# Kernel optimization log

Hardware: AMD Instinct MI355X
Metric: run time of the kernel (lower is better)

Reference implementation:

```python
import jax, jax.numpy as jnp
import numpy as np

L = 8          # fixed number of instance labels (0 = background), all assumed present
DV = 0.5       # delta_v
DD = 1.5       # delta_d
LOSS_WEIGHT = 1.0


def _safe_norm(x, axis):
    sq = jnp.sum(x * x, axis=axis)
    pos = sq > 0
    return jnp.sqrt(jnp.where(pos, sq, 1.0)) * pos.astype(x.dtype)


def _per_image(emb, inst, kern, tmask):
    # emb: [D,H,W], inst: [H,W] int, kern/tmask: [H,W] float
    D, H, W = emb.shape
    HW = H * W
    tm = (tmask > 0.5).astype(inst.dtype)
    kb = (kern > 0.5).astype(inst.dtype)
    inst = inst * tm
    inst_k = (inst * kb).reshape(-1)          # kernel-region labels
    inst_f = inst.reshape(-1)                 # full-region labels
    emb_f = emb.reshape(D, -1).T              # [HW, D]

    # --- generate_coef: first/second occurrence (row-major) of each label ---
    flat = jnp.arange(HW)
    eq = inst_f[None, :] == jnp.arange(L)[:, None]          # [L, HW]
    idxs = jnp.where(eq, flat[None, :], HW)
    first = jnp.min(idxs, axis=1)
    second = jnp.min(jnp.where(idxs == first[:, None], HW, idxs), axis=1)
    first = jnp.minimum(first, HW - 1)
    second = jnp.minimum(second, HW - 1)
    r0, c0 = first // W, first % W
    r1, c1 = second // W, second % W
    # pos_id = (tmp[0,0], tmp[1,0], tmp[0,-1], tmp[1,-1]) as in the source
    pos = jnp.stack([r0, r1, c0, c1], axis=1).astype(jnp.float32)  # [L,4]
    diag = jnp.sqrt(jnp.float32(H * H + W * W))
    coef_diag = jnp.exp(jnp.sqrt((pos[:, 0] - pos[:, 2]) ** 2 +
                                 (pos[:, 1] - pos[:, 3]) ** 2) / diag / 2.0)
    zmask = (jnp.arange(L) > 0).astype(jnp.float32)          # skip label 0
    coef_diag = coef_diag * zmask
    s = pos[:, 0] + pos[:, 2]
    t = pos[:, 1] + pos[:, 3]
    dp = jnp.sqrt((s[:, None] - s[None, :]) ** 2 + (t[:, None] - t[None, :]) ** 2)
    coef_off = 1.0 - 20.0 * jnp.exp(-4.0 - 2.5 * dp / diag)
    eye = jnp.eye(L, dtype=bool)
    coef = jnp.where(eye, coef_diag[:, None], coef_off)
    coef = coef * zmask[:, None] * zmask[None, :]

    # --- per-label kernel means (segment mean) ---
    ones = jnp.ones((HW,), jnp.float32)
    cnt_k = jax.ops.segment_sum(ones, inst_k, num_segments=L)
    mean = jax.ops.segment_sum(emb_f, inst_k, num_segments=L)
    mean = mean / jnp.maximum(cnt_k, 1.0)[:, None]           # [L, D]
    mean = mean * zmask[:, None]

    # --- l_agg: per-pixel distance to own-label mean, segment-mean per label ---
    mean_px = mean[inst_f]                                   # [HW, D] gather
    dist = _safe_norm(emb_f - mean_px, axis=1)
    cd_px = coef_diag[inst_f]
    val = jnp.log(jax.nn.relu(cd_px * dist - DV) ** 2 + 1.0)
    cnt = jax.ops.segment_sum(ones, inst_f, num_segments=L)
    l_agg_per = jax.ops.segment_sum(val, inst_f, num_segments=L) / jnp.maximum(cnt, 1.0)
    l_agg = jnp.mean(l_agg_per[1:])

    # --- l_dis: coefficient-weighted pairwise hinge between means ---
    Dn = _safe_norm(mean[:, None, :] - mean[None, :, :], axis=-1)  # [L, L]
    pm = (~eye) & (zmask[:, None] > 0) & (zmask[None, :] > 0)
    vals = jnp.log(jax.nn.relu(2.0 * DD - coef * Dn) ** 2 + 1.0)
    l_dis = jnp.sum(jnp.where(pm, vals, 0.0)) / ((L - 1) * (L - 2))

    # --- l_reg ---
    l_reg = jnp.mean(jnp.log(_safe_norm(mean, axis=1) + 1.0)) * 0.001
    return l_agg + l_dis + l_reg


def reference(emb, instance, kernel, training_mask, bboxes):
    # bboxes is accepted but unused, matching the original forward_single
    loss_batch = jax.vmap(_per_image)(emb, instance, kernel, training_mask)
    return LOSS_WEIGHT * jnp.mean(loss_batch)


def setup_inputs() -> dict:
    key = jax.random.key(0)
    k1, k2, k3, k4, k5 = jax.random.split(key, 5)
    B, D, H, W = 8, 4, 640, 640
    emb = jax.random.normal(k1, (B, D, H, W), dtype=jnp.float32)
    instance = jax.random.randint(k2, (B, H, W), 0, L, dtype=jnp.int32)
    kernel = jax.random.uniform(k3, (B, H, W), dtype=jnp.float32)
    training_mask = jax.random.uniform(k4, (B, H, W), dtype=jnp.float32)
    bboxes = jax.random.uniform(k5, (B, 10, 4), dtype=jnp.float32)
    return {"emb": emb, "instance": instance, "kernel": kernel,
            "training_mask": training_mask, "bboxes": bboxes}
```

## Files before the change

### kernel.cpp

```cpp
#include <hip/hip_runtime.h>

#define B_    8
#define D_    4
#define H_    640
#define W_    640
#define HW_   (H_ * W_)
#define L_    8
#define NL    (L_ - 1)
#define BLOCK 256
#define VITER 4
#define PXB   (BLOCK * 4 * VITER)
#define GRIDX (HW_ / PXB)

__device__ __forceinline__ void gatom_add(float* p, float v) {
    unsafeAtomicAdd(p, v);
}

__global__ void k_init(int* ib) {
    int t = threadIdx.x;
    if (t < 128) ib[t] = HW_;
    ib[128 + t] = 0;
    if (t < 137) ib[384 + t] = 0;
}

__global__ __attribute__((amdgpu_flat_work_group_size(BLOCK, BLOCK),
                          amdgpu_waves_per_eu(4, 8)))
void k_pass1(
        const float* __restrict__ emb, const int* __restrict__ inst,
        const float* __restrict__ kern, const float* __restrict__ tmask,
        int* __restrict__ firstIdx, int* __restrict__ secondIdx,
        int* __restrict__ cntf_i, int* __restrict__ cntk_i,
        float* __restrict__ sumemb, uint2* __restrict__ lblpack) {
    __shared__ int   sCnt[L_];
    __shared__ float sSum[L_ * D_];
    __shared__ int   sM1[L_], sM2[L_];

    const int tid  = threadIdx.x;
    const int lane = tid & 63;
    if (tid < L_) { sCnt[tid] = 0; sM1[tid] = HW_; sM2[tid] = HW_; }
    if (tid < L_ * D_) sSum[tid] = 0.f;
    __syncthreads();

    const int b = blockIdx.y;
    const int blockbase = blockIdx.x * PXB;
    const float* embb = emb + (size_t)b * D_ * HW_;
    const int base = b * HW_;
    const int o0 = blockbase + tid * 4;

    int4 LB[VITER]; float4 TM[VITER], KN[VITER];
    #pragma unroll
    for (int it = 0; it < VITER; ++it) {
        const int o = o0 + it * (BLOCK * 4);
        LB[it] = *(const int4*)  (inst  + base + o);
        TM[it] = *(const float4*)(tmask + base + o);
        KN[it] = *(const float4*)(kern  + base + o);
    }
    float4 E[2][2][D_];
    #pragma unroll
    for (int s = 0; s < 2; ++s)
        #pragma unroll
        for (int d = 0; d < D_; ++d)
            E[0][s][d] = *(const float4*)(embb + d * HW_ + o0 + s * (BLOCK * 4));

    int bp0 = 0, bp1 = 0, bp2 = 0, km = 0;
    unsigned int lpLo = 0, lpHi = 0;
    #pragma unroll
    for (int it = 0; it < VITER; ++it) {
        const int*   labA = (const int*)&LB[it];
        const float* tmA  = (const float*)&TM[it];
        const float* knA  = (const float*)&KN[it];
        #pragma unroll
        for (int c = 0; c < 4; ++c) {
            const int px = it * 4 + c;
            const int lf  = (tmA[c] > 0.5f) ? labA[c] : 0;
            const bool kb = (knA[c] > 0.5f);
            bp0 |= (lf & 1) << px;
            bp1 |= ((lf >> 1) & 1) << px;
            bp2 |= ((lf >> 2) & 1) << px;
            km  |= (kb ? 1 : 0) << px;
            if (px < 8) lpLo |= (unsigned int)lf << (4 * px);
            else        lpHi |= (unsigned int)lf << (4 * (px - 8));
        }
    }

    lblpack[(size_t)(b * GRIDX + blockIdx.x) * BLOCK + tid] = make_uint2(lpLo, lpHi);

    #pragma unroll
    for (int s = 0; s < 2; ++s)
        #pragma unroll
        for (int d = 0; d < D_; ++d)
            E[1][s][d] = *(const float4*)(embb + d * HW_ + o0 + (2 + s) * (BLOCK * 4));

    float sm[NL][D_];
    #pragma unroll
    for (int l = 0; l < NL; ++l)
        #pragma unroll
        for (int d = 0; d < D_; ++d) sm[l][d] = 0.f;

    #pragma unroll
    for (int half = 0; half < 2; ++half) {
        const unsigned int lp = half ? lpHi : lpLo;
        #pragma unroll
        for (int s = 0; s < 2; ++s) {
            const float* e0A = (const float*)&E[half][s][0];
            const float* e1A = (const float*)&E[half][s][1];
            const float* e2A = (const float*)&E[half][s][2];
            const float* e3A = (const float*)&E[half][s][3];
            #pragma unroll
            for (int c = 0; c < 4; ++c) {
                const int px  = half * 8 + s * 4 + c;
                const int nib = s * 4 + c;
                const int lf  = (int)((lp >> (4 * nib)) & 7u);
                const int lfk = ((km >> px) & 1) ? lf : 0;
                #pragma unroll
                for (int l = 1; l < L_; ++l) {
                    const float mk = (lfk == l) ? 1.0f : 0.0f;
                    sm[l - 1][0] += mk * e0A[c];
                    sm[l - 1][1] += mk * e1A[c];
                    sm[l - 1][2] += mk * e2A[c];
                    sm[l - 1][3] += mk * e3A[c];
                }
            }
        }
    }

    const int nb0 = ~bp0, nb1 = ~bp1, nb2 = ~bp2;
    int cnt[NL], m1[NL], m2[NL];
    #pragma unroll
    for (int l = 1; l < L_; ++l) {
        const int k = l - 1;
        int h = ((l & 1) ? bp0 : nb0) & ((l & 2) ? bp1 : nb1) & ((l & 4) ? bp2 : nb2);
        h &= 0xFFFF;
        cnt[k] = (__popc(h) << 16) | __popc(h & km);
        const int h2 = h & (h - 1);
        const int p1 = __ffs(h) - 1;
        const int p2 = __ffs(h2) - 1;
        m1[k] = h  ? (o0 + (p1 >> 2) * (BLOCK * 4) + (p1 & 3)) : HW_;
        m2[k] = h2 ? (o0 + (p2 >> 2) * (BLOCK * 4) + (p2 & 3)) : HW_;
    }

    #pragma unroll
    for (int l = 0; l < NL; ++l) {
        #pragma unroll
        for (int off = 32; off > 0; off >>= 1) {
            cnt[l]   += __shfl_down(cnt[l], off);
            sm[l][0] += __shfl_down(sm[l][0], off);
            sm[l][1] += __shfl_down(sm[l][1], off);
            sm[l][2] += __shfl_down(sm[l][2], off);
            sm[l][3] += __shfl_down(sm[l][3], off);
            int o1 = __shfl_down(m1[l], off);
            int o2 = __shfl_down(m2[l], off);
            m2[l] = min(min(m2[l], o2), max(m1[l], o1));
            m1[l] = min(m1[l], o1);
        }
    }
    if (lane == 0) {
        #pragma unroll
        for (int l = 0; l < NL; ++l) {
            atomicAdd(&sCnt[l + 1], cnt[l]);
            #pragma unroll
            for (int d = 0; d < D_; ++d) atomicAdd(&sSum[(l + 1) * D_ + d], sm[l][d]);
            int old = atomicMin(&sM1[l + 1], m1[l]);
            atomicMin(&sM2[l + 1], max(old, m1[l]));
            atomicMin(&sM2[l + 1], m2[l]);
        }
    }
    __syncthreads();

    if (tid >= 1 && tid < L_) {
        const int pc = sCnt[tid];
        atomicAdd(&cntf_i[b * L_ + tid], pc >> 16);
        atomicAdd(&cntk_i[b * L_ + tid], pc & 0xFFFF);
        int old = atomicMin(&firstIdx[b * L_ + tid], sM1[tid]);
        atomicMin(&secondIdx[b * L_ + tid], max(old, sM1[tid]));
        atomicMin(&secondIdx[b * L_ + tid], sM2[tid]);
    }
    if (tid >= D_ && tid < L_ * D_)
        gatom_add(&sumemb[b * L_ * D_ + tid], sSum[tid]);
}

__global__ __attribute__((amdgpu_flat_work_group_size(BLOCK, BLOCK),
                          amdgpu_waves_per_eu(4, 4)))
void k_pass3(
        const float* __restrict__ emb, const uint2* __restrict__ lblpack,
        const int* __restrict__ firstIdx, const int* __restrict__ secondIdx,
        const int* __restrict__ cntk_i, const int* __restrict__ cntf_i,
        const float* __restrict__ sumemb, float* __restrict__ sumvalb) {
    __shared__ float4 sMean[L_];
    __shared__ float  sCd[L_], sInv[L_];
    __shared__ float  sAcc;

    const int tid = threadIdx.x;
    const int b   = blockIdx.y;

    if (tid < L_) {
        float4 mu = {0.f, 0.f, 0.f, 0.f};
        float cd = 0.f, inv = 0.f;
        if (tid > 0) {
            const float invk = 1.0f / fmaxf((float)cntk_i[b * L_ + tid], 1.0f);
            mu.x = sumemb[b * L_ * D_ + tid * D_ + 0] * invk;
            mu.y = sumemb[b * L_ * D_ + tid * D_ + 1] * invk;
            mu.z = sumemb[b * L_ * D_ + tid * D_ + 2] * invk;
            mu.w = sumemb[b * L_ * D_ + tid * D_ + 3] * invk;
            const float diag = sqrtf((float)(H_ * H_ + W_ * W_));
            int f = min(firstIdx[b * L_ + tid],  HW_ - 1);
            int s = min(secondIdx[b * L_ + tid], HW_ - 1);
            float r0 = (float)(f / W_), c0 = (float)(f % W_);
            float r1 = (float)(s / W_), c1 = (float)(s % W_);
            cd = __expf(sqrtf((r0 - c0) * (r0 - c0) + (r1 - c1) * (r1 - c1))
                        / diag * 0.5f);
            inv = 1.0f / fmaxf((float)cntf_i[b * L_ + tid], 1.0f);
        }
        sMean[tid] = mu; sCd[tid] = cd; sInv[tid] = inv;
        if (tid == 0) sAcc = 0.f;
    }
    __syncthreads();

    const int blockbase = blockIdx.x * PXB;
    const float* embb = emb + (size_t)b * D_ * HW_;
    const int o0 = blockbase + tid * 4;

    const uint2 lp = lblpack[(size_t)(b * GRIDX + blockIdx.x) * BLOCK + tid];
    float4 E[VITER][D_];
    #pragma unroll
    for (int it = 0; it < VITER; ++it)
        #pragma unroll
        for (int d = 0; d < D_; ++d)
            E[it][d] = *(const float4*)(embb + d * HW_ + o0 + it * (BLOCK * 4));

    float acc = 0.f;
    #pragma unroll
    for (int it = 0; it < VITER; ++it) {
        const float* e0A = (const float*)&E[it][0];
        const float* e1A = (const float*)&E[it][1];
        const float* e2A = (const float*)&E[it][2];
        const float* e3A = (const float*)&E[it][3];
        #pragma unroll
        for (int c = 0; c < 4; ++c) {
            const int px = it * 4 + c;
            const int lf = (int)(((px < 8) ? (lp.x >> (4 * px))
                                           : (lp.y >> (4 * (px - 8)))) & 7u);
            const float4 mu = sMean[lf];
            float dx = e0A[c] - mu.x, dy = e1A[c] - mu.y;
            float dz = e2A[c] - mu.z, dw = e3A[c] - mu.w;
            float d2 = dx * dx + dy * dy + dz * dz + dw * dw;
            float x  = fmaxf(sCd[lf] * sqrtf(d2) - 0.5f, 0.0f);
            acc += __logf(x * x + 1.0f) * sInv[lf];
        }
    }

    #pragma unroll
    for (int off = 32; off > 0; off >>= 1)
        acc += __shfl_down(acc, off);
    if ((tid & 63) == 0) atomicAdd(&sAcc, acc);
    __syncthreads();
    if (tid == 0) gatom_add(&sumvalb[b], sAcc);
}

__global__ __launch_bounds__(512) void k_final(
        const int* __restrict__ firstIdx, const int* __restrict__ secondIdx,
        const int* __restrict__ cntk_i, const float* __restrict__ sumemb,
        const float* __restrict__ sumvalb, float* __restrict__ out) {
    __shared__ float sWave[8];
    const int tid = threadIdx.x;
    const int b = tid >> 6, ij = tid & 63, i = ij >> 3, j = ij & 7;
    const float diag = sqrtf((float)(H_ * H_ + W_ * W_));

    float mi[D_], mj[D_];
    {
        float ci = 1.0f / fmaxf((float)cntk_i[b * L_ + i], 1.0f);
        float cj = 1.0f / fmaxf((float)cntk_i[b * L_ + j], 1.0f);
        #pragma unroll
        for (int d = 0; d < D_; ++d) {
            mi[d] = (i > 0) ? sumemb[(b * L_ + i) * D_ + d] * ci : 0.0f;
            mj[d] = (j > 0) ? sumemb[(b * L_ + j) * D_ + d] * cj : 0.0f;
        }
    }

    float contrib = 0.0f;
    if (j == 0) {
        float d2 = 0.f;
        #pragma unroll
        for (int d = 0; d < D_; ++d) d2 += mi[d] * mi[d];
        float n = (d2 > 0.f) ? sqrtf(d2) : 0.f;
        contrib += __logf(n + 1.0f) * (0.001f / (float)L_);
    }
    if (i == 0 && j == 1)
        contrib += sumvalb[b] * (1.0f / (float)NL);
    if (i >= 1 && j >= 1 && i != j) {
        float d2 = 0.f;
        #pragma unroll
        for (int d = 0; d < D_; ++d) {
            float df = mi[d] - mj[d];
            d2 += df * df;
        }
        float Dn = (d2 > 0.f) ? sqrtf(d2) : 0.f;
        int fi = min(firstIdx[b * L_ + i],  HW_ - 1);
        int si = min(secondIdx[b * L_ + i], HW_ - 1);
        int fj = min(firstIdx[b * L_ + j],  HW_ - 1);
        int sj = min(secondIdx[b * L_ + j], HW_ - 1);
        float ssi = (float)(fi / W_) + (float)(fi % W_);
        float tti = (float)(si / W_) + (float)(si % W_);
        float ssj = (float)(fj / W_) + (float)(fj % W_);
        float ttj = (float)(sj / W_) + (float)(sj % W_);
        float dx = ssi - ssj, dy = tti - ttj;
        float dp = sqrtf(dx * dx + dy * dy);
        float coef = 1.0f - 20.0f * __expf(-4.0f - 2.5f * dp / diag);
        float x = fmaxf(3.0f - coef * Dn, 0.0f);
        contrib += __logf(x * x + 1.0f) * (1.0f / 42.0f);
    }

    #pragma unroll
    for (int off = 32; off > 0; off >>= 1)
        contrib += __shfl_down(contrib, off);
    if ((tid & 63) == 0) sWave[tid >> 6] = contrib;
    __syncthreads();
    if (tid == 0) {
        float t = 0.f;
        #pragma unroll
        for (int w = 0; w < 8; ++w) t += sWave[w];
        out[0] = t * (1.0f / (float)B_);
    }
}

extern "C" void kernel_launch(void* const* d_in, const int* in_sizes, int n_in,
                              void* d_out, int out_size, void* d_ws, size_t ws_size,
                              hipStream_t stream) {
    const float* emb   = (const float*)d_in[0];
    const int*   inst  = (const int*)  d_in[1];
    const float* kern  = (const float*)d_in[2];
    const float* tmask = (const float*)d_in[3];

    int*   ib        = (int*)d_ws;
    int*   firstIdx  = ib;
    int*   secondIdx = ib + 64;
    int*   cntf_i    = ib + 128;
    int*   cntk_i    = ib + 192;
    float* sumemb    = (float*)(ib + 256);
    float* sumvalb   = (float*)(ib + 512);
    uint2* lblpack   = (uint2*)(ib + 1024);
    float* out       = (float*)d_out;

    dim3 grid(GRIDX, B_);

    k_init <<<1, 256, 0, stream>>>(ib);
    k_pass1<<<grid, BLOCK, 0, stream>>>(emb, inst, kern, tmask,
                                        firstIdx, secondIdx, cntf_i, cntk_i,
                                        sumemb, lblpack);
    k_pass3<<<grid, BLOCK, 0, stream>>>(emb, lblpack, firstIdx, secondIdx,
                                        cntk_i, cntf_i, sumemb, sumvalb);
    k_final<<<1, 512, 0, stream>>>(firstIdx, secondIdx, cntk_i,
                                   sumemb, sumvalb, out);
}
```

Before: 148.0 us.

## Fuse both passes into one kernel with a per-image grid barrier

Merges the statistics pass and the pull-loss pass into a single kernel. Blocks of each image synchronise through a global atomic counter and flag, and each block keeps its embedding registers and packed labels across the barrier. This removes the second read of the embeddings, the label-pack buffer round trip and one kernel launch. In exchange it adds a software grid barrier that needs all 25 blocks per image (200 total) to be co-resident, plus spin-waiting and higher register pressure, and it adds scheduling barriers around the loads.

```diff
diff --git a/kernel.cpp b/kernel.cpp
--- a/kernel.cpp
+++ b/kernel.cpp
@@ -16,24 +16,35 @@
     unsafeAtomicAdd(p, v);
 }
 
+__device__ __forceinline__ int aload_i(const int* p) {
+    return __hip_atomic_load(p, __ATOMIC_ACQUIRE, __HIP_MEMORY_SCOPE_AGENT);
+}
+__device__ __forceinline__ float aload_f(const float* p) {
+    return __hip_atomic_load(p, __ATOMIC_ACQUIRE, __HIP_MEMORY_SCOPE_AGENT);
+}
+
 __global__ void k_init(int* ib) {
     int t = threadIdx.x;
     if (t < 128) ib[t] = HW_;
     ib[128 + t] = 0;
-    if (t < 137) ib[384 + t] = 0;
+    if (t < 176) ib[384 + t] = 0;
 }
 
 __global__ __attribute__((amdgpu_flat_work_group_size(BLOCK, BLOCK),
                           amdgpu_waves_per_eu(4, 8)))
-void k_pass1(
+void k_fused(
         const float* __restrict__ emb, const int* __restrict__ inst,
         const float* __restrict__ kern, const float* __restrict__ tmask,
         int* __restrict__ firstIdx, int* __restrict__ secondIdx,
         int* __restrict__ cntf_i, int* __restrict__ cntk_i,
-        float* __restrict__ sumemb, uint2* __restrict__ lblpack) {
-    __shared__ int   sCnt[L_];
-    __shared__ float sSum[L_ * D_];
-    __shared__ int   sM1[L_], sM2[L_];
+        float* __restrict__ sumemb, float* __restrict__ sumvalb,
+        int* __restrict__ barCnt, int* __restrict__ barFlag) {
+    __shared__ int    sCnt[L_];
+    __shared__ float  sSum[L_ * D_];
+    __shared__ int    sM1[L_], sM2[L_];
+    __shared__ float4 sMean[L_];
+    __shared__ float  sCd[L_], sInv[L_];
+    __shared__ float  sAcc;
 
     const int tid  = threadIdx.x;
     const int lane = tid & 63;
@@ -61,6 +72,7 @@
         #pragma unroll
         for (int d = 0; d < D_; ++d)
             E[0][s][d] = *(const float4*)(embb + d * HW_ + o0 + s * (BLOCK * 4));
+    __builtin_amdgcn_sched_barrier(0);
 
     int bp0 = 0, bp1 = 0, bp2 = 0, km = 0;
     unsigned int lpLo = 0, lpHi = 0;
@@ -83,13 +95,12 @@
         }
     }
 
-    lblpack[(size_t)(b * GRIDX + blockIdx.x) * BLOCK + tid] = make_uint2(lpLo, lpHi);
-
     #pragma unroll
     for (int s = 0; s < 2; ++s)
         #pragma unroll
         for (int d = 0; d < D_; ++d)
             E[1][s][d] = *(const float4*)(embb + d * HW_ + o0 + (2 + s) * (BLOCK * 4));
+    __builtin_amdgcn_sched_barrier(0);
 
     float sm[NL][D_];
     #pragma unroll
@@ -177,75 +188,67 @@
     }
     if (tid >= D_ && tid < L_ * D_)
         gatom_add(&sumemb[b * L_ * D_ + tid], sSum[tid]);
-}
-
-__global__ __attribute__((amdgpu_flat_work_group_size(BLOCK, BLOCK),
-                          amdgpu_waves_per_eu(4, 4)))
-void k_pass3(
-        const float* __restrict__ emb, const uint2* __restrict__ lblpack,
-        const int* __restrict__ firstIdx, const int* __restrict__ secondIdx,
-        const int* __restrict__ cntk_i, const int* __restrict__ cntf_i,
-        const float* __restrict__ sumemb, float* __restrict__ sumvalb) {
-    __shared__ float4 sMean[L_];
-    __shared__ float  sCd[L_], sInv[L_];
-    __shared__ float  sAcc;
-
-    const int tid = threadIdx.x;
-    const int b   = blockIdx.y;
+
+    __syncthreads();
+    if (tid == 0) {
+        __threadfence();
+        int prev = __hip_atomic_fetch_add(&barCnt[b], 1, __ATOMIC_ACQ_REL,
+                                          __HIP_MEMORY_SCOPE_AGENT);
+        if (prev == GRIDX - 1) {
+            __hip_atomic_store(&barFlag[b], 1, __ATOMIC_RELEASE,
+                               __HIP_MEMORY_SCOPE_AGENT);
+        } else {
+            while (__hip_atomic_load(&barFlag[b], __ATOMIC_ACQUIRE,
+                                     __HIP_MEMORY_SCOPE_AGENT) == 0)
+                __builtin_amdgcn_s_sleep(2);
+        }
+    }
+    __syncthreads();
 
     if (tid < L_) {
         float4 mu = {0.f, 0.f, 0.f, 0.f};
         float cd = 0.f, inv = 0.f;
         if (tid > 0) {
-            const float invk = 1.0f / fmaxf((float)cntk_i[b * L_ + tid], 1.0f);
-            mu.x = sumemb[b * L_ * D_ + tid * D_ + 0] * invk;
-            mu.y = sumemb[b * L_ * D_ + tid * D_ + 1] * invk;
-            mu.z = sumemb[b * L_ * D_ + tid * D_ + 2] * invk;
-            mu.w = sumemb[b * L_ * D_ + tid * D_ + 3] * invk;
+            const float invk = 1.0f / fmaxf((float)aload_i(&cntk_i[b * L_ + tid]), 1.0f);
+            mu.x = aload_f(&sumemb[b * L_ * D_ + tid * D_ + 0]) * invk;
+            mu.y = aload_f(&sumemb[b * L_ * D_ + tid * D_ + 1]) * invk;
+            mu.z = aload_f(&sumemb[b * L_ * D_ + tid * D_ + 2]) * invk;
+            mu.w = aload_f(&sumemb[b * L_ * D_ + tid * D_ + 3]) * invk;
             const float diag = sqrtf((float)(H_ * H_ + W_ * W_));
-            int f = min(firstIdx[b * L_ + tid],  HW_ - 1);
-            int s = min(secondIdx[b * L_ + tid], HW_ - 1);
+            int f = min(aload_i(&firstIdx[b * L_ + tid]),  HW_ - 1);
+            int s = min(aload_i(&secondIdx[b * L_ + tid]), HW_ - 1);
             float r0 = (float)(f / W_), c0 = (float)(f % W_);
             float r1 = (float)(s / W_), c1 = (float)(s % W_);
             cd = __expf(sqrtf((r0 - c0) * (r0 - c0) + (r1 - c1) * (r1 - c1))
                         / diag * 0.5f);
-            inv = 1.0f / fmaxf((float)cntf_i[b * L_ + tid], 1.0f);
+            inv = 1.0f / fmaxf((float)aload_i(&cntf_i[b * L_ + tid]), 1.0f);
         }
         sMean[tid] = mu; sCd[tid] = cd; sInv[tid] = inv;
         if (tid == 0) sAcc = 0.f;
     }
     __syncthreads();
 
-    const int blockbase = blockIdx.x * PXB;
-    const float* embb = emb + (size_t)b * D_ * HW_;
-    const int o0 = blockbase + tid * 4;
-
-    const uint2 lp = lblpack[(size_t)(b * GRIDX + blockIdx.x) * BLOCK + tid];
-    float4 E[VITER][D_];
-    #pragma unroll
-    for (int it = 0; it < VITER; ++it)
-        #pragma unroll
-        for (int d = 0; d < D_; ++d)
-            E[it][d] = *(const float4*)(embb + d * HW_ + o0 + it * (BLOCK * 4));
-
     float acc = 0.f;
     #pragma unroll
-    for (int it = 0; it < VITER; ++it) {
-        const float* e0A = (const float*)&E[it][0];
-        const float* e1A = (const float*)&E[it][1];
-        const float* e2A = (const float*)&E[it][2];
-        const float* e3A = (const float*)&E[it][3];
-        #pragma unroll
-        for (int c = 0; c < 4; ++c) {
-            const int px = it * 4 + c;
-            const int lf = (int)(((px < 8) ? (lp.x >> (4 * px))
-                                           : (lp.y >> (4 * (px - 8)))) & 7u);
-            const float4 mu = sMean[lf];
-            float dx = e0A[c] - mu.x, dy = e1A[c] - mu.y;
-            float dz = e2A[c] - mu.z, dw = e3A[c] - mu.w;
-            float d2 = dx * dx + dy * dy + dz * dz + dw * dw;
-            float x  = fmaxf(sCd[lf] * sqrtf(d2) - 0.5f, 0.0f);
-            acc += __logf(x * x + 1.0f) * sInv[lf];
+    for (int half = 0; half < 2; ++half) {
+        const unsigned int lp = half ? lpHi : lpLo;
+        #pragma unroll
+        for (int s = 0; s < 2; ++s) {
+            const float* e0A = (const float*)&E[half][s][0];
+            const float* e1A = (const float*)&E[half][s][1];
+            const float* e2A = (const float*)&E[half][s][2];
+            const float* e3A = (const float*)&E[half][s][3];
+            #pragma unroll
+            for (int c = 0; c < 4; ++c) {
+                const int nib = s * 4 + c;
+                const int lf  = (int)((lp >> (4 * nib)) & 7u);
+                const float4 mu = sMean[lf];
+                float dx = e0A[c] - mu.x, dy = e1A[c] - mu.y;
+                float dz = e2A[c] - mu.z, dw = e3A[c] - mu.w;
+                float d2 = dx * dx + dy * dy + dz * dz + dw * dw;
+                float x  = fmaxf(sCd[lf] * sqrtf(d2) - 0.5f, 0.0f);
+                acc += __logf(x * x + 1.0f) * sInv[lf];
+            }
         }
     }
 
@@ -338,17 +341,16 @@
     int*   cntk_i    = ib + 192;
     float* sumemb    = (float*)(ib + 256);
     float* sumvalb   = (float*)(ib + 512);
-    uint2* lblpack   = (uint2*)(ib + 1024);
+    int*   barCnt    = ib + 544;
+    int*   barFlag   = ib + 552;
     float* out       = (float*)d_out;
 
     dim3 grid(GRIDX, B_);
 
     k_init <<<1, 256, 0, stream>>>(ib);
-    k_pass1<<<grid, BLOCK, 0, stream>>>(emb, inst, kern, tmask,
+    k_fused<<<grid, BLOCK, 0, stream>>>(emb, inst, kern, tmask,
                                         firstIdx, secondIdx, cntf_i, cntk_i,
-                                        sumemb, lblpack);
-    k_pass3<<<grid, BLOCK, 0, stream>>>(emb, lblpack, firstIdx, secondIdx,
-                                        cntk_i, cntf_i, sumemb, sumvalb);
+                                        sumemb, sumvalb, barCnt, barFlag);
     k_final<<<1, 512, 0, stream>>>(firstIdx, secondIdx, cntk_i,
                                    sumemb, sumvalb, out);
 }
```

New measurement: 315.7 us. +113.3%, slower.

## Use inline-asm global loads with manual vmcnt waits to overlap loads and compute

Applied to the files above, without the earlier changes.

Replaces plain vector loads in both passes with inline-asm global_load instructions and explicit s_waitcnt vmcnt barriers. Label, mask and embedding loads can then be issued early and consumed in stages while later loads are still in flight. The second half of the embedding loads is issued before the first half's accumulation, and the lblpack store is moved after the accumulation. It also caps waves_per_eu at 4. Hand-counted vmcnt values are fragile: a miscount against the compiler's own memory ops would read data before it arrives, and sched_barrier blocks compiler rescheduling.

```diff
diff --git a/kernel.cpp b/kernel.cpp
--- a/kernel.cpp
+++ b/kernel.cpp
@@ -16,6 +16,24 @@
     unsafeAtomicAdd(p, v);
 }
 
+__device__ __forceinline__ float4 gload4f(const float* p) {
+    float4 r;
+    asm volatile("global_load_dwordx4 %0, %1, off" : "=v"(r) : "v"(p));
+    return r;
+}
+__device__ __forceinline__ int4 gload4i(const int* p) {
+    int4 r;
+    asm volatile("global_load_dwordx4 %0, %1, off" : "=v"(r) : "v"(p));
+    return r;
+}
+__device__ __forceinline__ uint2 gload2u(const uint2* p) {
+    uint2 r;
+    asm volatile("global_load_dwordx2 %0, %1, off" : "=v"(r) : "v"(p));
+    return r;
+}
+#define WAITCNT(n) asm volatile("s_waitcnt vmcnt(" #n ")"); \
+                   __builtin_amdgcn_sched_barrier(0)
+
 __global__ void k_init(int* ib) {
     int t = threadIdx.x;
     if (t < 128) ib[t] = HW_;
@@ -24,7 +42,7 @@
 }
 
 __global__ __attribute__((amdgpu_flat_work_group_size(BLOCK, BLOCK),
-                          amdgpu_waves_per_eu(4, 8)))
+                          amdgpu_waves_per_eu(4, 4)))
 void k_pass1(
         const float* __restrict__ emb, const int* __restrict__ inst,
         const float* __restrict__ kern, const float* __restrict__ tmask,
@@ -49,18 +67,22 @@
 
     int4 LB[VITER]; float4 TM[VITER], KN[VITER];
     #pragma unroll
-    for (int it = 0; it < VITER; ++it) {
-        const int o = o0 + it * (BLOCK * 4);
-        LB[it] = *(const int4*)  (inst  + base + o);
-        TM[it] = *(const float4*)(tmask + base + o);
-        KN[it] = *(const float4*)(kern  + base + o);
-    }
-    float4 E[2][2][D_];
+    for (int it = 0; it < VITER; ++it)
+        LB[it] = gload4i(inst + base + o0 + it * (BLOCK * 4));
+    #pragma unroll
+    for (int it = 0; it < VITER; ++it)
+        TM[it] = gload4f(tmask + base + o0 + it * (BLOCK * 4));
+    #pragma unroll
+    for (int it = 0; it < VITER; ++it)
+        KN[it] = gload4f(kern + base + o0 + it * (BLOCK * 4));
+    float4 E0[2][D_];
     #pragma unroll
     for (int s = 0; s < 2; ++s)
         #pragma unroll
         for (int d = 0; d < D_; ++d)
-            E[0][s][d] = *(const float4*)(embb + d * HW_ + o0 + s * (BLOCK * 4));
+            E0[s][d] = gload4f(embb + d * HW_ + o0 + s * (BLOCK * 4));
+
+    WAITCNT(8);
 
     int bp0 = 0, bp1 = 0, bp2 = 0, km = 0;
     unsigned int lpLo = 0, lpHi = 0;
@@ -83,46 +105,69 @@
         }
     }
 
+    float4 E1[2][D_];
+    #pragma unroll
+    for (int s = 0; s < 2; ++s)
+        #pragma unroll
+        for (int d = 0; d < D_; ++d)
+            E1[s][d] = gload4f(embb + d * HW_ + o0 + (2 + s) * (BLOCK * 4));
+
+    WAITCNT(8);
+
+    float sm[NL][D_];
+    #pragma unroll
+    for (int l = 0; l < NL; ++l)
+        #pragma unroll
+        for (int d = 0; d < D_; ++d) sm[l][d] = 0.f;
+
+    #pragma unroll
+    for (int s = 0; s < 2; ++s) {
+        const float* e0A = (const float*)&E0[s][0];
+        const float* e1A = (const float*)&E0[s][1];
+        const float* e2A = (const float*)&E0[s][2];
+        const float* e3A = (const float*)&E0[s][3];
+        #pragma unroll
+        for (int c = 0; c < 4; ++c) {
+            const int px  = s * 4 + c;
+            const int lf  = (int)((lpLo >> (4 * px)) & 7u);
+            const int lfk = ((km >> px) & 1) ? lf : 0;
+            #pragma unroll
+            for (int l = 1; l < L_; ++l) {
+                const float mk = (lfk == l) ? 1.0f : 0.0f;
+                sm[l - 1][0] += mk * e0A[c];
+                sm[l - 1][1] += mk * e1A[c];
+                sm[l - 1][2] += mk * e2A[c];
+                sm[l - 1][3] += mk * e3A[c];
+            }
+        }
+    }
+
+    WAITCNT(0);
+
+    #pragma unroll
+    for (int s = 0; s < 2; ++s) {
+        const float* e0A = (const float*)&E1[s][0];
+        const float* e1A = (const float*)&E1[s][1];
+        const float* e2A = (const float*)&E1[s][2];
+        const float* e3A = (const float*)&E1[s][3];
+        #pragma unroll
+        for (int c = 0; c < 4; ++c) {
+            const int px  = 8 + s * 4 + c;
+            const int nib = s * 4 + c;
+            const int lf  = (int)((lpHi >> (4 * nib)) & 7u);
+            const int lfk = ((km >> px) & 1) ? lf : 0;
+            #pragma unroll
+            for (int l = 1; l < L_; ++l) {
+                const float mk = (lfk == l) ? 1.0f : 0.0f;
+                sm[l - 1][0] += mk * e0A[c];
+                sm[l - 1][1] += mk * e1A[c];
+                sm[l - 1][2] += mk * e2A[c];
+                sm[l - 1][3] += mk * e3A[c];
+            }
+        }
+    }
+
     lblpack[(size_t)(b * GRIDX + blockIdx.x) * BLOCK + tid] = make_uint2(lpLo, lpHi);
-
-    #pragma unroll
-    for (int s = 0; s < 2; ++s)
-        #pragma unroll
-        for (int d = 0; d < D_; ++d)
-            E[1][s][d] = *(const float4*)(embb + d * HW_ + o0 + (2 + s) * (BLOCK * 4));
-
-    float sm[NL][D_];
-    #pragma unroll
-    for (int l = 0; l < NL; ++l)
-        #pragma unroll
-        for (int d = 0; d < D_; ++d) sm[l][d] = 0.f;
-
-    #pragma unroll
-    for (int half = 0; half < 2; ++half) {
-        const unsigned int lp = half ? lpHi : lpLo;
-        #pragma unroll
-        for (int s = 0; s < 2; ++s) {
-            const float* e0A = (const float*)&E[half][s][0];
-            const float* e1A = (const float*)&E[half][s][1];
-            const float* e2A = (const float*)&E[half][s][2];
-            const float* e3A = (const float*)&E[half][s][3];
-            #pragma unroll
-            for (int c = 0; c < 4; ++c) {
-                const int px  = half * 8 + s * 4 + c;
-                const int nib = s * 4 + c;
-                const int lf  = (int)((lp >> (4 * nib)) & 7u);
-                const int lfk = ((km >> px) & 1) ? lf : 0;
-                #pragma unroll
-                for (int l = 1; l < L_; ++l) {
-                    const float mk = (lfk == l) ? 1.0f : 0.0f;
-                    sm[l - 1][0] += mk * e0A[c];
-                    sm[l - 1][1] += mk * e1A[c];
-                    sm[l - 1][2] += mk * e2A[c];
-                    sm[l - 1][3] += mk * e3A[c];
-                }
-            }
-        }
-    }
 
     const int nb0 = ~bp0, nb1 = ~bp1, nb2 = ~bp2;
     int cnt[NL], m1[NL], m2[NL];
@@ -220,17 +265,22 @@
     const float* embb = emb + (size_t)b * D_ * HW_;
     const int o0 = blockbase + tid * 4;
 
-    const uint2 lp = lblpack[(size_t)(b * GRIDX + blockIdx.x) * BLOCK + tid];
+    const uint2 lp = gload2u(lblpack + (size_t)(b * GRIDX + blockIdx.x) * BLOCK + tid);
     float4 E[VITER][D_];
     #pragma unroll
     for (int it = 0; it < VITER; ++it)
         #pragma unroll
         for (int d = 0; d < D_; ++d)
-            E[it][d] = *(const float4*)(embb + d * HW_ + o0 + it * (BLOCK * 4));
+            E[it][d] = gload4f(embb + d * HW_ + o0 + it * (BLOCK * 4));
 
     float acc = 0.f;
     #pragma unroll
     for (int it = 0; it < VITER; ++it) {
+        if (it == 0) { WAITCNT(12); }
+        else if (it == 1) { WAITCNT(8); }
+        else if (it == 2) { WAITCNT(4); }
+        else { WAITCNT(0); }
+
         const float* e0A = (const float*)&E[it][0];
         const float* e1A = (const float*)&E[it][1];
         const float* e2A = (const float*)&E[it][2];
```

New measurement: 149.2 us. No clear change (+0.8%).
